# Kernel tuning notes

Measured on AMD Instinct MI355X. Metric: run time of the kernel, lower is better.

Reference implementation:

```python
import jax, jax.numpy as jnp
import numpy as np

WIN = 11  # hard-coded window size in the original module

def sinusoidal_pe(L, D):
    pos = jnp.arange(L, dtype=jnp.float32)[:, None]
    div = jnp.exp(jnp.arange(0, D, 2, dtype=jnp.float32) * (-np.log(10000.0) / D))
    pe = jnp.zeros((L, D), dtype=jnp.float32)
    pe = pe.at[:, 0::2].set(jnp.sin(pos * div))
    pe = pe.at[:, 1::2].set(jnp.cos(pos * div))
    return pe


def setup_inputs() -> dict:
    key = jax.random.key(0)
    ks = jax.random.split(key, 6)
    B, Lq, Ld, D, V = 16, 30, 1100, 768, 50000
    return {
        "q": jax.random.randint(ks[0], (B, Lq), 0, V),
        "d_pos": jax.random.randint(ks[1], (B, Ld), 0, V),
        "d_neg": jax.random.randint(ks[2], (B, Ld), 0, V),
        "q_mask": jnp.ones((B, Lq, 1), jnp.float32),
        "d_pos_mask": jnp.ones((B, Ld, 1), jnp.float32),
        "d_neg_mask": jnp.ones((B, Ld, 1), jnp.float32),
        "pe_flag": 1,
        "emb_table": jax.random.normal(ks[3], (V, D), jnp.float32) * 0.02,
        "W_lin": jax.random.normal(ks[4], (D, D), jnp.float32) * 0.02,
        "W_out": jax.random.normal(ks[5], (D, D), jnp.float32) * 0.02,
    }


def reference(q, d_pos, d_neg, q_mask, d_pos_mask, d_neg_mask, pe_flag, emb_table, W_lin, W_out):
    B, Lq = q.shape
    Ld = d_pos.shape[1]
    D = emb_table.shape[1]
    H = 12
    Dh = D // H
    W_num = Ld // WIN  # number of 11-token windows

    qe = emb_table[q] * q_mask              # [B,Lq,D]
    dp = emb_table[d_pos]                   # [B,Ld,D]
    dn = emb_table[d_neg]
    if pe_flag:
        pe = sinusoidal_pe(Ld, D)[None]     # [1,Ld,D]
        scale_emb = jnp.sqrt(jnp.float32(D))
        dp = dp * scale_emb + pe            # dropout p=0 -> identity
        dn = dn * scale_emb + pe
    dp = dp * d_pos_mask
    dn = dn * d_neg_mask

    dp = dp.reshape(B, W_num, WIN, D)       # [B,W,11,D]
    dn = dn.reshape(B, W_num, WIN, D)
    qx = jnp.broadcast_to(qe[:, None], (B, W_num, Lq, D))  # expand over windows

    # linear_trans (no bias): y = x @ W_lin.T
    queries = jnp.einsum('bwqd,ed->bwqe', qx, W_lin)
    dp = jnp.einsum('bwkd,ed->bwke', dp, W_lin)
    dn = jnp.einsum('bwkd,ed->bwke', dn, W_lin)

    # faithful replication of torch .view head-split: pure reshape, mixes seq+channel
    def split(x, L):
        return x.reshape(B, W_num, H, L, Dh)

    queries = split(queries, Lq) * (Dh ** -0.5)

    def attend(doc):
        d = split(doc, WIN)                                  # [B,W,H,11,Dh]
        logits = jnp.einsum('bwhqd,bwhkd->bwhqk', queries, d)
        weights = jax.nn.softmax(logits, axis=-1)            # dropout p=0
        ctx = jnp.einsum('bwhqk,bwhkd->bwhqd', weights, d)
        ctx = ctx.reshape(B, W_num, Lq, D)                   # faithful merge (.view)
        return jnp.einsum('bwqd,ed->bwqe', ctx, W_out)

    return attend(dp), attend(dn)
```

## Files before the change

### kernel.cpp

```cpp
#include <hip/hip_runtime.h>
#include <hip/hip_bf16.h>
#include <cstdint>
#include <cstddef>

#define B_    16
#define LQ    30
#define LD    1100
#define DIM   768
#define NH    12
#define DH_   64
#define WINSZ 11
#define WNUM  100
#define NSLOT 32

typedef __attribute__((ext_vector_type(8))) short short8;
typedef __attribute__((ext_vector_type(4))) float f32x4;

__device__ __forceinline__ void gload_lds16(const void* g, void* l) {
  __builtin_amdgcn_global_load_lds(
      (const __attribute__((address_space(1))) void*)g,
      (__attribute__((address_space(3))) void*)l, 16, 0, 0);
}

__global__ __launch_bounds__(256) void wconv_kernel(const float* __restrict__ wa,
    const float* __restrict__ wb, __hip_bfloat16* __restrict__ oa,
    __hip_bfloat16* __restrict__ ob) {
  int i = (blockIdx.x * 256 + threadIdx.x) * 4;
  if (i >= DIM * DIM) return;
  float4 va = *reinterpret_cast<const float4*>(wa + i);
  float4 vb = *reinterpret_cast<const float4*>(wb + i);
  union { __hip_bfloat16 h[4]; uint2 u; } pa, pb;
  pa.h[0] = __float2bfloat16(va.x); pa.h[1] = __float2bfloat16(va.y);
  pa.h[2] = __float2bfloat16(va.z); pa.h[3] = __float2bfloat16(va.w);
  pb.h[0] = __float2bfloat16(vb.x); pb.h[1] = __float2bfloat16(vb.y);
  pb.h[2] = __float2bfloat16(vb.z); pb.h[3] = __float2bfloat16(vb.w);
  *reinterpret_cast<uint2*>(oa + i) = pa.u;
  *reinterpret_cast<uint2*>(ob + i) = pb.u;
}

__global__ __launch_bounds__(256) void prep_q_kernel(const int* __restrict__ q,
    const float* __restrict__ qmask, const float* __restrict__ emb,
    __hip_bfloat16* __restrict__ Xq) {
  int idx = blockIdx.x * 256 + threadIdx.x;
  if (idx >= B_ * LQ * (DIM / 4)) return;
  int row = idx / (DIM / 4);
  int c4  = idx % (DIM / 4);
  float m = qmask[row] * 0.125f;
  float4 v = *reinterpret_cast<const float4*>(emb + (size_t)q[row] * DIM + c4 * 4);
  union { __hip_bfloat16 h[4]; uint2 u; } o;
  o.h[0] = __float2bfloat16(v.x * m); o.h[1] = __float2bfloat16(v.y * m);
  o.h[2] = __float2bfloat16(v.z * m); o.h[3] = __float2bfloat16(v.w * m);
  *reinterpret_cast<uint2*>(Xq + (size_t)row * DIM + c4 * 4) = o.u;
}

__global__ __launch_bounds__(256) void prep_d_kernel(const int* __restrict__ dpos,
    const int* __restrict__ dneg, const float* __restrict__ dpmask,
    const float* __restrict__ dnmask, const float* __restrict__ emb,
    const int* __restrict__ peflag, __hip_bfloat16* __restrict__ X,
    int s0, int rows) {
  int idx = blockIdx.x * 256 + threadIdx.x;
  if (idx >= rows * (DIM / 4)) return;
  int r  = idx / (DIM / 4);
  int c4 = idx % (DIM / 4);
  int s = s0 + r / LD;
  int t = r % LD;
  int doc = s >> 4, b = s & 15;
  const int*   di = doc ? dneg   : dpos;
  const float* dm = doc ? dnmask : dpmask;
  int grow = b * LD + t;
  float m = dm[grow];
  float4 v = *reinterpret_cast<const float4*>(emb + (size_t)di[grow] * DIM + c4 * 4);
  if (peflag[0]) {
    int i0 = c4 * 2;
    float d0 = expf(-0.023985261387f * (float)i0);
    float d1 = expf(-0.023985261387f * (float)(i0 + 1));
    float s0f, c0f, s1f, c1f;
    sincosf((float)t * d0, &s0f, &c0f);
    sincosf((float)t * d1, &s1f, &c1f);
    v.x = v.x * 27.712812921102035f + s0f;
    v.y = v.y * 27.712812921102035f + c0f;
    v.z = v.z * 27.712812921102035f + s1f;
    v.w = v.w * 27.712812921102035f + c1f;
  }
  union { __hip_bfloat16 h[4]; uint2 u; } o;
  o.h[0] = __float2bfloat16(v.x * m); o.h[1] = __float2bfloat16(v.y * m);
  o.h[2] = __float2bfloat16(v.z * m); o.h[3] = __float2bfloat16(v.w * m);
  *reinterpret_cast<uint2*>(X + (size_t)r * DIM + c4 * 4) = o.u;
}

template <bool OUT_BF16>
__global__ __launch_bounds__(512, 2) void gemm_mfma(const __hip_bfloat16* __restrict__ A,
    const __hip_bfloat16* __restrict__ Bt, void* __restrict__ Cv,
    int M, int N, int K, int tilesX, int tiles1,
    const __hip_bfloat16* __restrict__ A2, float* __restrict__ C2, int M2) {
  extern __shared__ __hip_bfloat16 smem[];
  __hip_bfloat16* As = smem;
  __hip_bfloat16* Bs = smem + 4 * 8192;

  const int nwg  = gridDim.x;
  const int orig = blockIdx.x;
  const int q8 = nwg >> 3, r8 = nwg & 7;
  const int xcd = orig & 7, pos = orig >> 3;
  const int wgid = (xcd < r8 ? xcd * (q8 + 1) : r8 * (q8 + 1) + (xcd - r8) * q8) + pos;

  const bool is2 = (wgid >= tiles1);
  const int  w2  = is2 ? (wgid - tiles1) : wgid;
  const int row0 = (w2 / tilesX) * 256;
  const int col0 = (w2 % tilesX) * 256;
  const __hip_bfloat16* Ap = is2 ? A2 : A;
  const int Mloc = is2 ? M2 : M;

  const int tid  = threadIdx.x;
  const int lane = tid & 63;
  const int wave = tid >> 6;
  const int wr = wave >> 2, wc = wave & 3;
  const int lo4 = lane & 15;
  const int hi4 = lane >> 4;

  const int csrc = (tid & 3) ^ ((tid >> 3) & 3);
  const __hip_bfloat16* gA = Ap + (size_t)(row0 + (tid >> 2)) * K + csrc * 8;
  const __hip_bfloat16* gB = Bt + (size_t)(col0 + (tid >> 2)) * K + csrc * 8;

  const int coff = ((hi4 ^ ((lo4 >> 1) & 3)) * 8);
  const int arow = (wr * 128 + lo4) * 32 + coff;
  const int brow = (wc * 64  + lo4) * 32 + coff;

  f32x4 acc[8][4] = {};

  auto STAGE = [&](int tt) {
    const int k0 = tt * 32;
    const int lo = (tt & 3) * 8192;
    gload_lds16(gA + k0,                   As + lo + tid * 8);
    gload_lds16(gA + (size_t)128 * K + k0, As + lo + 4096 + tid * 8);
    gload_lds16(gB + k0,                   Bs + lo + tid * 8);
    gload_lds16(gB + (size_t)128 * K + k0, Bs + lo + 4096 + tid * 8);
  };

#define MFMA4(MB)                                                       \
    _Pragma("unroll")                                                   \
    for (int n = 0; n < 4; ++n)                                         \
      acc[MB][n] = __builtin_amdgcn_mfma_f32_16x16x32_bf16(             \
          bq[n], af0, acc[MB][n], 0, 0, 0);                             \
    _Pragma("unroll")                                                   \
    for (int n = 0; n < 4; ++n)                                         \
      acc[MB + 1][n] = __builtin_amdgcn_mfma_f32_16x16x32_bf16(         \
          bq[n], af1, acc[MB + 1][n], 0, 0, 0);

#define STEP(tt, WAITN, DOSTAGE)                                        \
  {                                                                     \
    const int lo = ((tt) & 3) * 8192;                                   \
    const int so = (((tt) + 3) & 3) * 8192;                             \
    const int k0s = ((tt) + 3) * 32;                                    \
    const __hip_bfloat16* Ab = As + lo + arow;                          \
    const __hip_bfloat16* Bb = Bs + lo + brow;                          \
    short8 bq[4], af0, af1, af2, af3;                                   \
                                                 \
    asm volatile("s_waitcnt vmcnt(" WAITN ")" ::: "memory");            \
    __builtin_amdgcn_s_barrier();                                       \
    __builtin_amdgcn_sched_barrier(0);                                  \
    bq[0] = *reinterpret_cast<const short8*>(Bb);                       \
    bq[1] = *reinterpret_cast<const short8*>(Bb + 512);                 \
    bq[2] = *reinterpret_cast<const short8*>(Bb + 1024);                \
    bq[3] = *reinterpret_cast<const short8*>(Bb + 1536);                \
    af0 = *reinterpret_cast<const short8*>(Ab);                         \
    af1 = *reinterpret_cast<const short8*>(Ab + 512);                   \
    af2 = *reinterpret_cast<const short8*>(Ab + 1024);                  \
    af3 = *reinterpret_cast<const short8*>(Ab + 1536);                  \
    if (DOSTAGE) {                                                      \
      gload_lds16(gA + k0s,                   As + so + tid * 8);       \
      gload_lds16(gA + (size_t)128 * K + k0s, As + so + 4096 + tid * 8);\
    }                                                                   \
    asm volatile("s_waitcnt lgkmcnt(0)" ::: "memory");                  \
    __builtin_amdgcn_sched_barrier(0);                                  \
    __builtin_amdgcn_s_setprio(1);                                      \
    MFMA4(0)                                                            \
    { short8 t0 = af2, t1 = af3; af0 = t0; af1 = t1; }                  \
    MFMA4(2)                                                            \
    __builtin_amdgcn_s_setprio(0);                                      \
                                                 \
    __builtin_amdgcn_s_barrier();                                       \
    af0 = *reinterpret_cast<const short8*>(Ab + 2048);                  \
    af1 = *reinterpret_cast<const short8*>(Ab + 2560);                  \
    af2 = *reinterpret_cast<const short8*>(Ab + 3072);                  \
    af3 = *reinterpret_cast<const short8*>(Ab + 3584);                  \
    if (DOSTAGE) {                                                      \
      gload_lds16(gB + k0s,                   Bs + so + tid * 8);       \
      gload_lds16(gB + (size_t)128 * K + k0s, Bs + so + 4096 + tid * 8);\
    }                                                                   \
    asm volatile("s_waitcnt lgkmcnt(0)" ::: "memory");                  \
    __builtin_amdgcn_sched_barrier(0);                                  \
    __builtin_amdgcn_s_setprio(1);                                      \
    MFMA4(4)                                                            \
    { short8 t0 = af2, t1 = af3; af0 = t0; af1 = t1; }                  \
    MFMA4(6)                                                            \
    __builtin_amdgcn_s_setprio(0);                                      \
  }

  const int nt = K / 32;
  STAGE(0); STAGE(1); STAGE(2);
  for (int t = 0; t < nt - 3; ++t)
    STEP(t, "8", true)
  STEP(nt - 3, "8", false)
  STEP(nt - 2, "4", false)
  STEP(nt - 1, "0", false)
#undef STEP
#undef MFMA4

#pragma unroll
  for (int m = 0; m < 8; ++m) {
    const int r = row0 + wr * 128 + m * 16 + lo4;
    if (r < Mloc) {
#pragma unroll
      for (int n = 0; n < 4; ++n) {
        const int cb = col0 + wc * 64 + n * 16 + hi4 * 4;
        f32x4 v = acc[m][n];
        if (is2) {
          *reinterpret_cast<f32x4*>(C2 + (size_t)r * N + cb) = v;
        } else if constexpr (OUT_BF16) {
          union { __hip_bfloat16 h[4]; uint2 u; } p;
          p.h[0] = __float2bfloat16(v[0]); p.h[1] = __float2bfloat16(v[1]);
          p.h[2] = __float2bfloat16(v[2]); p.h[3] = __float2bfloat16(v[3]);
          *reinterpret_cast<uint2*>((__hip_bfloat16*)Cv + (size_t)r * N + cb) = p.u;
        } else {
          *reinterpret_cast<f32x4*>((float*)Cv + (size_t)r * N + cb) = v;
        }
      }
    }
  }
}

__global__ __launch_bounds__(128) void attn_kernel(const float* __restrict__ Qs,
    const __hip_bfloat16* __restrict__ Y, __hip_bfloat16* __restrict__ ctx, int s0) {
  int blk = blockIdx.x;
  int h  = blk % NH;
  int w  = (blk / NH) % WNUM;
  int sl = blk / (NH * WNUM);
  int b  = (s0 + sl) & 15;

  __shared__ float Dl[WINSZ][DH_];

  const __hip_bfloat16* Yb = Y + ((size_t)(sl * LD + w * WINSZ)) * DIM + h * (WINSZ * DH_);
  const float* Qb = Qs + (size_t)b * (LQ * DIM) + h * (LQ * DH_);

  int tid = threadIdx.x;
  int qi = tid >> 2, part = tid & 3;

  if (tid < 88) {
    uint4 raw = *reinterpret_cast<const uint4*>(Yb + tid * 8);
    const __hip_bfloat16* hp = reinterpret_cast<const __hip_bfloat16*>(&raw);
    float* dst = &Dl[0][0] + tid * 8;
#pragma unroll
    for (int j = 0; j < 8; ++j) dst[j] = __bfloat162float(hp[j]);
  }

  float4 qreg[4];
#pragma unroll
  for (int j = 0; j < 4; ++j)
    qreg[j] = *reinterpret_cast<const float4*>(Qb + qi * DH_ + part * 16 + j * 4);
  __syncthreads();

  float dot[WINSZ];
#pragma unroll
  for (int k = 0; k < WINSZ; ++k) {
    const float4* dp = reinterpret_cast<const float4*>(&Dl[k][part * 16]);
    float s = 0.f;
#pragma unroll
    for (int j = 0; j < 4; ++j) {
      float4 dv = dp[j];
      s += qreg[j].x * dv.x + qreg[j].y * dv.y + qreg[j].z * dv.z + qreg[j].w * dv.w;
    }
    dot[k] = s;
  }
#pragma unroll
  for (int k = 0; k < WINSZ; ++k) {
    dot[k] += __shfl_xor(dot[k], 1);
    dot[k] += __shfl_xor(dot[k], 2);
  }
  float mx = -1e30f;
#pragma unroll
  for (int k = 0; k < WINSZ; ++k) mx = fmaxf(mx, dot[k]);
  float sum = 0.f;
#pragma unroll
  for (int k = 0; k < WINSZ; ++k) { dot[k] = expf(dot[k] - mx); sum += dot[k]; }
  float inv = 1.f / sum;

  float4 o[4] = {};
#pragma unroll
  for (int k = 0; k < WINSZ; ++k) {
    float pk = dot[k];
    const float4* dp = reinterpret_cast<const float4*>(&Dl[k][part * 16]);
#pragma unroll
    for (int j = 0; j < 4; ++j) {
      float4 dv = dp[j];
      o[j].x += pk * dv.x; o[j].y += pk * dv.y;
      o[j].z += pk * dv.z; o[j].w += pk * dv.w;
    }
  }
  union { __hip_bfloat16 hh[16]; uint4 v[2]; } pk;
#pragma unroll
  for (int j = 0; j < 4; ++j) {
    pk.hh[j * 4 + 0] = __float2bfloat16(o[j].x * inv);
    pk.hh[j * 4 + 1] = __float2bfloat16(o[j].y * inv);
    pk.hh[j * 4 + 2] = __float2bfloat16(o[j].z * inv);
    pk.hh[j * 4 + 3] = __float2bfloat16(o[j].w * inv);
  }
  __hip_bfloat16* op = ctx + (size_t)(sl * WNUM + w) * (LQ * DIM)
                     + h * (LQ * DH_) + qi * DH_ + part * 16;
  *reinterpret_cast<uint4*>(op)     = pk.v[0];
  *reinterpret_cast<uint4*>(op + 8) = pk.v[1];
}

extern "C" void kernel_launch(void* const* d_in, const int* in_sizes, int n_in,
                              void* d_out, int out_size, void* d_ws, size_t ws_size,
                              hipStream_t stream) {
  const int*   q      = (const int*)d_in[0];
  const int*   dpos   = (const int*)d_in[1];
  const int*   dneg   = (const int*)d_in[2];
  const float* qmask  = (const float*)d_in[3];
  const float* dpmask = (const float*)d_in[4];
  const float* dnmask = (const float*)d_in[5];
  const int*   peflag = (const int*)d_in[6];
  const float* emb    = (const float*)d_in[7];
  const float* Wlin   = (const float*)d_in[8];
  const float* Wout   = (const float*)d_in[9];
  float* out = (float*)d_out;

  (void)hipFuncSetAttribute(reinterpret_cast<const void*>(&gemm_mfma<false>),
                            hipFuncAttributeMaxDynamicSharedMemorySize, 131072);
  (void)hipFuncSetAttribute(reinterpret_cast<const void*>(&gemm_mfma<true>),
                            hipFuncAttributeMaxDynamicSharedMemorySize, 131072);

  char* ws = (char*)d_ws;
  size_t off = 0;
  auto alloc = [&](size_t bytes) -> char* {
    char* p = ws + off; off += (bytes + 255) & ~(size_t)255; return p;
  };
  __hip_bfloat16* Xq   = (__hip_bfloat16*)alloc((size_t)512 * DIM * 2);
  float*          Qsc  = (float*)         alloc((size_t)B_ * LQ * DIM * 4);
  __hip_bfloat16* Wl16 = (__hip_bfloat16*)alloc((size_t)DIM * DIM * 2);
  __hip_bfloat16* Wo16 = (__hip_bfloat16*)alloc((size_t)DIM * DIM * 2);

  int SC = NSLOT;
  while (SC > 1) {
    size_t need = off
        + ((size_t)SC * LD + 256) * DIM * 2 * 2
        + ((size_t)SC * WNUM * LQ + 256) * DIM * 2 + (1u << 20);
    if (need <= ws_size) break;
    SC >>= 1;
  }
  __hip_bfloat16* X   = (__hip_bfloat16*)alloc(((size_t)SC * LD + 256) * DIM * 2);
  __hip_bfloat16* Y   = (__hip_bfloat16*)alloc(((size_t)SC * LD + 256) * DIM * 2);
  __hip_bfloat16* ctx = (__hip_bfloat16*)alloc(((size_t)SC * WNUM * LQ + 256) * DIM * 2);

  wconv_kernel<<<(DIM * DIM / 4 + 255) / 256, 256, 0, stream>>>(Wlin, Wout, Wl16, Wo16);
  prep_q_kernel<<<(B_ * LQ * (DIM / 4) + 255) / 256, 256, 0, stream>>>(q, qmask, emb, Xq);

  const int tilesX = DIM / 256;
  const int qTiles = tilesX * ((B_ * LQ + 255) / 256);

  for (int s0 = 0; s0 < NSLOT; s0 += SC) {
    const int rowsX = SC * LD;
    const int rowsC = SC * WNUM * LQ;
    prep_d_kernel<<<(rowsX * (DIM / 4) + 255) / 256, 256, 0, stream>>>(
        dpos, dneg, dpmask, dnmask, emb, peflag, X, s0, rowsX);
    {
      int tiles1 = tilesX * ((rowsX + 255) / 256);
      int t2 = (s0 == 0) ? qTiles : 0;
      gemm_mfma<true><<<tiles1 + t2, 512, 131072, stream>>>(
          X, Wl16, Y, rowsX, DIM, DIM, tilesX, tiles1, Xq, Qsc, B_ * LQ);
    }
    attn_kernel<<<SC * WNUM * NH, 120, 0, stream>>>(Qsc, Y, ctx, s0);
    {
      int tiles1 = tilesX * ((rowsC + 255) / 256);
      gemm_mfma<false><<<tiles1, 512, 131072, stream>>>(
          ctx, Wo16, out + (size_t)s0 * WNUM * LQ * DIM, rowsC, DIM, DIM,
          tilesX, tiles1, nullptr, nullptr, 0);
    }
  }
}
```

Baseline: 385.4 us.

## Shrink GEMM tile to 128x256 with triple-buffered LDS and higher occupancy

Reworks the bf16 MFMA GEMM from 256x256 tiles with a 4-stage LDS ring to 128x256 tiles with a 3-stage ring. Each of the 8 waves now owns a 128x32 output slice instead of a 128x64 one. LDS drops from 128 KB to 72 KB and launch bounds rise to 4 blocks per CU, aiming for more resident workgroups and a finer grid. The cost is less operand reuse per tile, more total A/B traffic, and a shallower prefetch pipeline.

```diff
diff --git a/kernel.cpp b/kernel.cpp
--- a/kernel.cpp
+++ b/kernel.cpp
@@ -89,13 +89,13 @@
 }
 
 template <bool OUT_BF16>
-__global__ __launch_bounds__(512, 2) void gemm_mfma(const __hip_bfloat16* __restrict__ A,
+__global__ __launch_bounds__(512, 4) void gemm_mfma(const __hip_bfloat16* __restrict__ A,
     const __hip_bfloat16* __restrict__ Bt, void* __restrict__ Cv,
     int M, int N, int K, int tilesX, int tiles1,
     const __hip_bfloat16* __restrict__ A2, float* __restrict__ C2, int M2) {
   extern __shared__ __hip_bfloat16 smem[];
   __hip_bfloat16* As = smem;
-  __hip_bfloat16* Bs = smem + 4 * 8192;
+  __hip_bfloat16* Bs = smem + 3 * 4096;
 
   const int nwg  = gridDim.x;
   const int orig = blockIdx.x;
@@ -105,15 +105,14 @@
 
   const bool is2 = (wgid >= tiles1);
   const int  w2  = is2 ? (wgid - tiles1) : wgid;
-  const int row0 = (w2 / tilesX) * 256;
+  const int row0 = (w2 / tilesX) * 128;
   const int col0 = (w2 % tilesX) * 256;
   const __hip_bfloat16* Ap = is2 ? A2 : A;
   const int Mloc = is2 ? M2 : M;
 
   const int tid  = threadIdx.x;
   const int lane = tid & 63;
-  const int wave = tid >> 6;
-  const int wr = wave >> 2, wc = wave & 3;
+  const int wc   = tid >> 6;
   const int lo4 = lane & 15;
   const int hi4 = lane >> 4;
 
@@ -121,61 +120,53 @@
   const __hip_bfloat16* gA = Ap + (size_t)(row0 + (tid >> 2)) * K + csrc * 8;
   const __hip_bfloat16* gB = Bt + (size_t)(col0 + (tid >> 2)) * K + csrc * 8;
 
-  const int coff = ((hi4 ^ ((lo4 >> 1) & 3)) * 8);
-  const int arow = (wr * 128 + lo4) * 32 + coff;
-  const int brow = (wc * 64  + lo4) * 32 + coff;
-
-  f32x4 acc[8][4] = {};
+  const int coff = (hi4 ^ ((lo4 >> 1) & 3)) * 8;
+  const int arow = lo4 * 32 + coff;
+  const int brow = (wc * 32 + lo4) * 32 + coff;
+
+  f32x4 acc[8][2] = {};
 
   auto STAGE = [&](int tt) {
     const int k0 = tt * 32;
-    const int lo = (tt & 3) * 8192;
-    gload_lds16(gA + k0,                   As + lo + tid * 8);
-    gload_lds16(gA + (size_t)128 * K + k0, As + lo + 4096 + tid * 8);
-    gload_lds16(gB + k0,                   Bs + lo + tid * 8);
-    gload_lds16(gB + (size_t)128 * K + k0, Bs + lo + 4096 + tid * 8);
+    const int b3 = tt % 3;
+    gload_lds16(gA + k0,                   As + b3 * 4096 + tid * 8);
+    gload_lds16(gB + k0,                   Bs + b3 * 8192 + tid * 8);
+    gload_lds16(gB + (size_t)128 * K + k0, Bs + b3 * 8192 + 4096 + tid * 8);
   };
 
-#define MFMA4(MB)                                                       \
-    _Pragma("unroll")                                                   \
-    for (int n = 0; n < 4; ++n)                                         \
-      acc[MB][n] = __builtin_amdgcn_mfma_f32_16x16x32_bf16(             \
-          bq[n], af0, acc[MB][n], 0, 0, 0);                             \
-    _Pragma("unroll")                                                   \
-    for (int n = 0; n < 4; ++n)                                         \
-      acc[MB + 1][n] = __builtin_amdgcn_mfma_f32_16x16x32_bf16(         \
-          bq[n], af1, acc[MB + 1][n], 0, 0, 0);
+#define MFMA2(MB)                                                       \
+    acc[MB][0] = __builtin_amdgcn_mfma_f32_16x16x32_bf16(               \
+        bq0, af0, acc[MB][0], 0, 0, 0);                                 \
+    acc[MB][1] = __builtin_amdgcn_mfma_f32_16x16x32_bf16(               \
+        bq1, af0, acc[MB][1], 0, 0, 0);                                 \
+    acc[MB + 1][0] = __builtin_amdgcn_mfma_f32_16x16x32_bf16(           \
+        bq0, af1, acc[MB + 1][0], 0, 0, 0);                             \
+    acc[MB + 1][1] = __builtin_amdgcn_mfma_f32_16x16x32_bf16(           \
+        bq1, af1, acc[MB + 1][1], 0, 0, 0);
 
 #define STEP(tt, WAITN, DOSTAGE)                                        \
   {                                                                     \
-    const int lo = ((tt) & 3) * 8192;                                   \
-    const int so = (((tt) + 3) & 3) * 8192;                             \
-    const int k0s = ((tt) + 3) * 32;                                    \
-    const __hip_bfloat16* Ab = As + lo + arow;                          \
-    const __hip_bfloat16* Bb = Bs + lo + brow;                          \
-    short8 bq[4], af0, af1, af2, af3;                                   \
+    const int b3 = (tt) % 3;                                            \
+    const __hip_bfloat16* Ab = As + b3 * 4096 + arow;                   \
+    const __hip_bfloat16* Bb = Bs + b3 * 8192 + brow;                   \
+    short8 bq0, bq1, af0, af1, af2, af3;                                \
                                                  \
     asm volatile("s_waitcnt vmcnt(" WAITN ")" ::: "memory");            \
     __builtin_amdgcn_s_barrier();                                       \
     __builtin_amdgcn_sched_barrier(0);                                  \
-    bq[0] = *reinterpret_cast<const short8*>(Bb);                       \
-    bq[1] = *reinterpret_cast<const short8*>(Bb + 512);                 \
-    bq[2] = *reinterpret_cast<const short8*>(Bb + 1024);                \
-    bq[3] = *reinterpret_cast<const short8*>(Bb + 1536);                \
+    bq0 = *reinterpret_cast<const short8*>(Bb);                         \
+    bq1 = *reinterpret_cast<const short8*>(Bb + 512);                   \
     af0 = *reinterpret_cast<const short8*>(Ab);                         \
     af1 = *reinterpret_cast<const short8*>(Ab + 512);                   \
     af2 = *reinterpret_cast<const short8*>(Ab + 1024);                  \
     af3 = *reinterpret_cast<const short8*>(Ab + 1536);                  \
-    if (DOSTAGE) {                                                      \
-      gload_lds16(gA + k0s,                   As + so + tid * 8);       \
-      gload_lds16(gA + (size_t)128 * K + k0s, As + so + 4096 + tid * 8);\
-    }                                                                   \
+    if (DOSTAGE) STAGE((tt) + 2);                                       \
     asm volatile("s_waitcnt lgkmcnt(0)" ::: "memory");                  \
     __builtin_amdgcn_sched_barrier(0);                                  \
     __builtin_amdgcn_s_setprio(1);                                      \
-    MFMA4(0)                                                            \
+    MFMA2(0)                                                            \
     { short8 t0 = af2, t1 = af3; af0 = t0; af1 = t1; }                  \
-    MFMA4(2)                                                            \
+    MFMA2(2)                                                            \
     __builtin_amdgcn_s_setprio(0);                                      \
                                                  \
     __builtin_amdgcn_s_barrier();                                       \
@@ -183,36 +174,31 @@
     af1 = *reinterpret_cast<const short8*>(Ab + 2560);                  \
     af2 = *reinterpret_cast<const short8*>(Ab + 3072);                  \
     af3 = *reinterpret_cast<const short8*>(Ab + 3584);                  \
-    if (DOSTAGE) {                                                      \
-      gload_lds16(gB + k0s,                   Bs + so + tid * 8);       \
-      gload_lds16(gB + (size_t)128 * K + k0s, Bs + so + 4096 + tid * 8);\
-    }                                                                   \
     asm volatile("s_waitcnt lgkmcnt(0)" ::: "memory");                  \
     __builtin_amdgcn_sched_barrier(0);                                  \
     __builtin_amdgcn_s_setprio(1);                                      \
-    MFMA4(4)                                                            \
+    MFMA2(4)                                                            \
     { short8 t0 = af2, t1 = af3; af0 = t0; af1 = t1; }                  \
-    MFMA4(6)                                                            \
+    MFMA2(6)                                                            \
     __builtin_amdgcn_s_setprio(0);                                      \
   }
 
   const int nt = K / 32;
-  STAGE(0); STAGE(1); STAGE(2);
-  for (int t = 0; t < nt - 3; ++t)
-    STEP(t, "8", true)
-  STEP(nt - 3, "8", false)
-  STEP(nt - 2, "4", false)
+  STAGE(0); STAGE(1);
+  for (int t = 0; t < nt - 2; ++t)
+    STEP(t, "3", true)
+  STEP(nt - 2, "3", false)
   STEP(nt - 1, "0", false)
 #undef STEP
-#undef MFMA4
+#undef MFMA2
 
 #pragma unroll
   for (int m = 0; m < 8; ++m) {
-    const int r = row0 + wr * 128 + m * 16 + lo4;
+    const int r = row0 + m * 16 + lo4;
     if (r < Mloc) {
 #pragma unroll
-      for (int n = 0; n < 4; ++n) {
-        const int cb = col0 + wc * 64 + n * 16 + hi4 * 4;
+      for (int n = 0; n < 2; ++n) {
+        const int cb = col0 + wc * 32 + n * 16 + hi4 * 4;
         f32x4 v = acc[m][n];
         if (is2) {
           *reinterpret_cast<f32x4*>(C2 + (size_t)r * N + cb) = v;
@@ -325,10 +311,11 @@
   const float* Wout   = (const float*)d_in[9];
   float* out = (float*)d_out;
 
+  const int LDS_BYTES = 3 * 4096 * 2 + 3 * 8192 * 2;
   (void)hipFuncSetAttribute(reinterpret_cast<const void*>(&gemm_mfma<false>),
-                            hipFuncAttributeMaxDynamicSharedMemorySize, 131072);
+                            hipFuncAttributeMaxDynamicSharedMemorySize, LDS_BYTES);
   (void)hipFuncSetAttribute(reinterpret_cast<const void*>(&gemm_mfma<true>),
-                            hipFuncAttributeMaxDynamicSharedMemorySize, 131072);
+                            hipFuncAttributeMaxDynamicSharedMemorySize, LDS_BYTES);
 
   char* ws = (char*)d_ws;
   size_t off = 0;
@@ -343,20 +330,20 @@
   int SC = NSLOT;
   while (SC > 1) {
     size_t need = off
-        + ((size_t)SC * LD + 256) * DIM * 2 * 2
-        + ((size_t)SC * WNUM * LQ + 256) * DIM * 2 + (1u << 20);
+        + ((size_t)SC * LD + 128) * DIM * 2 * 2
+        + ((size_t)SC * WNUM * LQ + 128) * DIM * 2 + (1u << 20);
     if (need <= ws_size) break;
     SC >>= 1;
   }
-  __hip_bfloat16* X   = (__hip_bfloat16*)alloc(((size_t)SC * LD + 256) * DIM * 2);
-  __hip_bfloat16* Y   = (__hip_bfloat16*)alloc(((size_t)SC * LD + 256) * DIM * 2);
-  __hip_bfloat16* ctx = (__hip_bfloat16*)alloc(((size_t)SC * WNUM * LQ + 256) * DIM * 2);
+  __hip_bfloat16* X   = (__hip_bfloat16*)alloc(((size_t)SC * LD + 128) * DIM * 2);
+  __hip_bfloat16* Y   = (__hip_bfloat16*)alloc(((size_t)SC * LD + 128) * DIM * 2);
+  __hip_bfloat16* ctx = (__hip_bfloat16*)alloc(((size_t)SC * WNUM * LQ + 128) * DIM * 2);
 
   wconv_kernel<<<(DIM * DIM / 4 + 255) / 256, 256, 0, stream>>>(Wlin, Wout, Wl16, Wo16);
   prep_q_kernel<<<(B_ * LQ * (DIM / 4) + 255) / 256, 256, 0, stream>>>(q, qmask, emb, Xq);
 
   const int tilesX = DIM / 256;
-  const int qTiles = tilesX * ((B_ * LQ + 255) / 256);
+  const int qTiles = tilesX * ((B_ * LQ + 127) / 128);
 
   for (int s0 = 0; s0 < NSLOT; s0 += SC) {
     const int rowsX = SC * LD;
@@ -364,15 +351,15 @@
     prep_d_kernel<<<(rowsX * (DIM / 4) + 255) / 256, 256, 0, stream>>>(
         dpos, dneg, dpmask, dnmask, emb, peflag, X, s0, rowsX);
     {
-      int tiles1 = tilesX * ((rowsX + 255) / 256);
+      int tiles1 = tilesX * ((rowsX + 127) / 128);
       int t2 = (s0 == 0) ? qTiles : 0;
-      gemm_mfma<true><<<tiles1 + t2, 512, 131072, stream>>>(
+      gemm_mfma<true><<<tiles1 + t2, 512, LDS_BYTES, stream>>>(
           X, Wl16, Y, rowsX, DIM, DIM, tilesX, tiles1, Xq, Qsc, B_ * LQ);
     }
     attn_kernel<<<SC * WNUM * NH, 120, 0, stream>>>(Qsc, Y, ctx, s0);
     {
-      int tiles1 = tilesX * ((rowsC + 255) / 256);
-      gemm_mfma<false><<<tiles1, 512, 131072, stream>>>(
+      int tiles1 = tilesX * ((rowsC + 127) / 128);
+      gemm_mfma<false><<<tiles1, 512, LDS_BYTES, stream>>>(
           ctx, Wo16, out + (size_t)s0 * WNUM * LQ * DIM, rowsC, DIM, DIM,
           tilesX, tiles1, nullptr, nullptr, 0);
     }
```

Result: slower. 406.9 us (+5.6%).
